# Performance work log

Hardware: AMD Instinct MI355X
Metric: run time of the kernel (lower is better)

The kernel has to match this reference:

```python
import jax, jax.numpy as jnp
import numpy as np

N = 200000
C = 256
C4 = C // 4
K = 27
B = 8
EPS = 1e-5


def setup_inputs() -> dict:
    key = jax.random.key(0)
    ks = jax.random.split(key, 16)
    s = 0.02
    inp = {
        "x": jax.random.normal(ks[0], (N, C), jnp.float32),
        "nbr6": jax.random.randint(ks[1], (N, K), 0, N + 1).astype(jnp.int32),
        "nbr12": jax.random.randint(ks[2], (N, K), 0, N + 1).astype(jnp.int32),
        "nbr18": jax.random.randint(ks[3], (N, K), 0, N + 1).astype(jnp.int32),
        "batch_idx": jnp.sort(jax.random.randint(ks[4], (N,), 0, B)).astype(jnp.int32),
        # 1x1 convs = plain matmul
        "W1": jax.random.normal(ks[5], (C, C4), jnp.float32) * s,
        "b1": jnp.zeros((C4,), jnp.float32),
        # 3^3 sparse convs: weight per kernel offset
        "W6": jax.random.normal(ks[6], (K, C, C4), jnp.float32) * s,
        "b6": jnp.zeros((C4,), jnp.float32),
        "W12": jax.random.normal(ks[7], (K, C, C4), jnp.float32) * s,
        "b12": jnp.zeros((C4,), jnp.float32),
        "W18": jax.random.normal(ks[8], (K, C, C4), jnp.float32) * s,
        "b18": jnp.zeros((C4,), jnp.float32),
        "W5": jax.random.normal(ks[9], (C, C4), jnp.float32) * s,
        "b5": jnp.zeros((C4,), jnp.float32),
        "Wc": jax.random.normal(ks[10], (5 * C4, C), jnp.float32) * s,
        "bc": jnp.zeros((C,), jnp.float32),
    }
    for i in range(1, 6):
        inp[f"g{i}"] = jnp.ones((C4,), jnp.float32)
        inp[f"be{i}"] = jnp.zeros((C4,), jnp.float32)
    inp["gc"] = jnp.ones((C,), jnp.float32)
    inp["bec"] = jnp.zeros((C,), jnp.float32)
    return inp


def _bn(x, g, b):
    # training-mode batch norm over the point dimension
    m = jnp.mean(x, axis=0)
    v = jnp.var(x, axis=0)
    return (x - m) * jax.lax.rsqrt(v + EPS) * g + b


def _sparse_conv(x, nbr, W, b):
    # gather-GEMM-scatter: x [N,C], nbr [N,K] in [0,N] (N = missing), W [K,C,Co]
    xp = jnp.concatenate([x, jnp.zeros((1, x.shape[1]), x.dtype)], axis=0)

    def step(acc, kin):
        nk, Wk = kin  # nk [N], Wk [C,Co]
        return acc + xp[nk] @ Wk, None

    init = jnp.zeros((x.shape[0], W.shape[2]), x.dtype)
    acc, _ = jax.lax.scan(step, init, (nbr.T, W))
    return acc + b


def _pool_broadcast(x, batch_idx):
    # global average pool per point cloud, broadcast back to points
    s = jax.ops.segment_sum(x, batch_idx, num_segments=B)
    cnt = jax.ops.segment_sum(jnp.ones((x.shape[0], 1), x.dtype), batch_idx, num_segments=B)
    mean = s / jnp.maximum(cnt, 1.0)
    return mean[batch_idx]


def reference(x, nbr6, nbr12, nbr18, batch_idx,
              W1, b1, W6, b6, W12, b12, W18, b18, W5, b5, Wc, bc,
              g1, be1, g2, be2, g3, be3, g4, be4, g5, be5, gc, bec):
    relu = jax.nn.relu
    x1 = relu(_bn(x @ W1 + b1, g1, be1))
    x2 = relu(_bn(_sparse_conv(x, nbr6, W6, b6), g2, be2))
    x3 = relu(_bn(_sparse_conv(x, nbr12, W12, b12), g3, be3))
    x4 = relu(_bn(_sparse_conv(x, nbr18, W18, b18), g4, be4))
    x5 = _pool_broadcast(x, batch_idx)
    x5 = relu(_bn(x5 @ W5 + b5, g5, be5))
    x6 = jnp.concatenate([x1, x2, x3, x4, x5], axis=1)
    x6 = relu(_bn(x6 @ Wc + bc, gc, bec))
    return x6 + x
```

## Files before the change

### kernel.cpp

```cpp
#include <hip/hip_runtime.h>

#define N_PTS 200000
#define KNBR 27
#define EPS_BN 1e-5f

typedef __attribute__((ext_vector_type(8))) short short8;
typedef __attribute__((ext_vector_type(4))) float f32x4;

#define WS_POOL_SUM   0u
#define WS_POOL_CNT   8192u
#define WS_BR_SUM     8448u
#define WS_BR_SQ      9472u
#define WS_C_SUM      10496u
#define WS_C_SQ       11520u
#define WS_ZROW       12544u
#define WS_A_BR       16384u
#define WS_D_BR       17408u
#define WS_AC         18432u
#define WS_DC         19456u
#define WS_R5         20480u
#define WS_WT1        24576u
#define WS_WTC        57344u
#define WS_WT6        221184u
#define WS_WT12       1105920u
#define WS_WT18       1990656u
#define WS_Y          3145728u
#define Y_STRIDE      12800000u

__device__ __forceinline__ float bf2f(unsigned short u) {
  union { unsigned int i; float f; } c; c.i = ((unsigned int)u) << 16; return c.f;
}
__device__ __forceinline__ unsigned short f2bf(float f) {
  union { float f; unsigned int i; } c; c.f = f;
  unsigned int u = c.i;
  u += 0x7fffu + ((u >> 16) & 1u);
  return (unsigned short)(u >> 16);
}
__device__ __forceinline__ short8 load8bf(const unsigned short* p) {
  return *(const short8*)p;
}

__global__ __launch_bounds__(256) void init_zero(float* __restrict__ p) {
  p[blockIdx.x * 256 + threadIdx.x] = 0.f;
}

__global__ __launch_bounds__(256) void cvt_x(
    const float* __restrict__ x, unsigned short* __restrict__ xb)
{
  size_t e = ((size_t)blockIdx.x * 256 + threadIdx.x) * 8;
  const size_t lim = (size_t)N_PTS * 256;
  if (e >= lim) {
    if (e < lim + 256) {
      short8 z = {0, 0, 0, 0, 0, 0, 0, 0};
      *(short8*)(xb + e) = z;
    }
    return;
  }
  const float4* q4 = (const float4*)(x + e);
  float4 a = q4[0], b = q4[1];
  short8 r;
  r[0] = (short)f2bf(a.x); r[1] = (short)f2bf(a.y);
  r[2] = (short)f2bf(a.z); r[3] = (short)f2bf(a.w);
  r[4] = (short)f2bf(b.x); r[5] = (short)f2bf(b.y);
  r[6] = (short)f2bf(b.z); r[7] = (short)f2bf(b.w);
  *(short8*)(xb + e) = r;
}

__global__ __launch_bounds__(256) void prep_weights(
    const float* __restrict__ W6, const float* __restrict__ W12,
    const float* __restrict__ W18, const float* __restrict__ W1,
    const float* __restrict__ Wc, char* __restrict__ ws)
{
  int slice = blockIdx.x;
  const float* src; unsigned short* dst; int R, C;
  if (slice < 27)      { src = W6  + slice * 16384;        dst = (unsigned short*)(ws + WS_WT6)  + slice * 16384;        R = 256; C = 64; }
  else if (slice < 54) { src = W12 + (slice - 27) * 16384; dst = (unsigned short*)(ws + WS_WT12) + (slice - 27) * 16384; R = 256; C = 64; }
  else if (slice < 81) { src = W18 + (slice - 54) * 16384; dst = (unsigned short*)(ws + WS_WT18) + (slice - 54) * 16384; R = 256; C = 64; }
  else if (slice == 81){ src = W1;  dst = (unsigned short*)(ws + WS_WT1); R = 256; C = 64; }
  else                 { src = Wc;  dst = (unsigned short*)(ws + WS_WTC); R = 320; C = 256; }
  int total = R * C;
  for (int e = threadIdx.x; e < total; e += 256) {
    int r = e / C, c = e - r * C;
    dst[c * R + r] = f2bf(src[e]);
  }
}

__global__ __launch_bounds__(256) void pool_kernel(
    const float* __restrict__ x, const int* __restrict__ bidx,
    float* __restrict__ pool_sum, float* __restrict__ pool_cnt)
{
  int c = threadIdx.x;
  int base = blockIdx.x * 256;
  int end = base + 256; if (end > N_PTS) end = N_PTS;
  float acc = 0.f, cnt = 0.f; int cur = -1;
  for (int row = base; row < end; ++row) {
    int b = bidx[row];
    if (b != cur) {
      if (cur >= 0) {
        atomicAdd(pool_sum + cur * 256 + c, acc);
        if (c == 0) atomicAdd(pool_cnt + cur, cnt);
      }
      acc = 0.f; cnt = 0.f; cur = b;
    }
    acc += x[(size_t)row * 256 + c];
    cnt += 1.f;
  }
  if (cur >= 0) {
    atomicAdd(pool_sum + cur * 256 + c, acc);
    if (c == 0) atomicAdd(pool_cnt + cur, cnt);
  }
}

__global__ __launch_bounds__(256) void conv_mfma(
    const unsigned short* __restrict__ xb,
    const int* __restrict__ nbr6, const int* __restrict__ nbr12,
    const int* __restrict__ nbr18, char* __restrict__ ws)
{
  const int conv = blockIdx.y;
  const int* nbr = (conv == 1) ? nbr6 : (conv == 2) ? nbr12 : (conv == 3) ? nbr18 : nullptr;
  const unsigned short* Wt = (const unsigned short*)(ws +
      (conv == 0 ? WS_WT1 : conv == 1 ? WS_WT6 : conv == 2 ? WS_WT12 : WS_WT18));
  const int kcount = conv ? KNBR : 1;
  unsigned short* yout = (unsigned short*)(ws + WS_Y) + (size_t)conv * Y_STRIDE;
  float* sum_out = (float*)(ws + WS_BR_SUM) + conv * 64;
  float* sq_out  = (float*)(ws + WS_BR_SQ)  + conv * 64;

  const int tid = threadIdx.x;
  const int wave = tid >> 6, lane = tid & 63;
  const int m = lane & 15, q = lane >> 4;
  const int base = blockIdx.x * 256 + wave * 64;

  f32x4 zero4 = {0.f, 0.f, 0.f, 0.f};
  f32x4 acc[4][4];
  #pragma unroll
  for (int a = 0; a < 4; ++a)
    #pragma unroll
    for (int b = 0; b < 4; ++b) acc[a][b] = zero4;

  int rows[4]; bool valid[4];
  #pragma unroll
  for (int ms = 0; ms < 4; ++ms) {
    rows[ms] = base + ms * 16 + m;
    valid[ms] = rows[ms] < N_PTS;
  }

  int idxc[4];
  #pragma unroll
  for (int ms = 0; ms < 4; ++ms)
    idxc[ms] = valid[ms] ? (nbr ? nbr[rows[ms] * KNBR] : rows[ms]) : N_PTS;

  #pragma unroll 1
  for (int k = 0; k < kcount; ++k) {
    int idxn[4];
    #pragma unroll
    for (int ms = 0; ms < 4; ++ms)
      idxn[ms] = (k + 1 < kcount && valid[ms]) ? nbr[rows[ms] * KNBR + k + 1] : N_PTS;

    const unsigned short* wk = Wt + (size_t)k * 16384;
    const unsigned short* ap[4];
    #pragma unroll
    for (int ms = 0; ms < 4; ++ms) ap[ms] = xb + (size_t)idxc[ms] * 256;

    #pragma unroll
    for (int cc = 0; cc < 8; ++cc) {
      const int c0 = cc * 32 + q * 8;
      short8 af[4], bfr[4];
      #pragma unroll
      for (int ms = 0; ms < 4; ++ms) af[ms] = load8bf(ap[ms] + c0);
      #pragma unroll
      for (int t = 0; t < 4; ++t) bfr[t] = load8bf(wk + (t * 16 + m) * 256 + c0);
      #pragma unroll
      for (int ms = 0; ms < 4; ++ms)
        #pragma unroll
        for (int t = 0; t < 4; ++t)
          acc[ms][t] = __builtin_amdgcn_mfma_f32_16x16x32_bf16(af[ms], bfr[t], acc[ms][t], 0, 0, 0);
    }
    #pragma unroll
    for (int ms = 0; ms < 4; ++ms) idxc[ms] = idxn[ms];
  }

  #pragma unroll
  for (int t = 0; t < 4; ++t) {
    float s = 0.f, s2 = 0.f;
    #pragma unroll
    for (int ms = 0; ms < 4; ++ms)
      #pragma unroll
      for (int r = 0; r < 4; ++r) { float v = acc[ms][t][r]; s += v; s2 += v * v; }
    s  += __shfl_xor(s, 16);  s  += __shfl_xor(s, 32);
    s2 += __shfl_xor(s2, 16); s2 += __shfl_xor(s2, 32);
    if (lane < 16) {
      atomicAdd(sum_out + t * 16 + lane, s);
      atomicAdd(sq_out  + t * 16 + lane, s2);
    }
  }

  #pragma unroll
  for (int ms = 0; ms < 4; ++ms) {
    #pragma unroll
    for (int r = 0; r < 4; ++r) {
      int row = base + ms * 16 + q * 4 + r;
      if (row < N_PTS) {
        #pragma unroll
        for (int t = 0; t < 4; ++t)
          yout[(size_t)row * 64 + t * 16 + m] = f2bf(acc[ms][t][r]);
      }
    }
  }
}

__global__ __launch_bounds__(256) void finalize_branch(
    char* __restrict__ ws,
    const float* __restrict__ g1, const float* __restrict__ be1,
    const float* __restrict__ g2, const float* __restrict__ be2,
    const float* __restrict__ g3, const float* __restrict__ be3,
    const float* __restrict__ g4, const float* __restrict__ be4,
    const float* __restrict__ g5, const float* __restrict__ be5,
    const float* __restrict__ W5)
{
  __shared__ float y5s[8][64];
  __shared__ float a5s[64], d5s[64];
  const int tid = threadIdx.x;
  float* pool_sum = (float*)(ws + WS_POOL_SUM);
  float* pool_cnt = (float*)(ws + WS_POOL_CNT);
  float* br_sum = (float*)(ws + WS_BR_SUM);
  float* br_sq  = (float*)(ws + WS_BR_SQ);
  float* a_br   = (float*)(ws + WS_A_BR);
  float* d_br   = (float*)(ws + WS_D_BR);
  unsigned short* r5 = (unsigned short*)(ws + WS_R5);

  {
    int conv = tid >> 6, co = tid & 63;
    const float* gp[4] = {g1, g2, g3, g4};
    const float* bp[4] = {be1, be2, be3, be4};
    float mean = br_sum[tid] / (float)N_PTS;
    float var = fmaxf(br_sq[tid] / (float)N_PTS - mean * mean, 0.f);
    float a = gp[conv][co] * rsqrtf(var + EPS_BN);
    a_br[tid] = a;
    d_br[tid] = bp[conv][co] - mean * a;
  }
  {
    int co = tid & 63, b0 = tid >> 6;
    for (int b = b0; b < 8; b += 4) {
      float inv = 1.f / fmaxf(pool_cnt[b], 1.f);
      float acc = 0.f;
      for (int c = 0; c < 256; ++c)
        acc += pool_sum[b * 256 + c] * inv * W5[c * 64 + co];
      y5s[b][co] = acc;
    }
  }
  __syncthreads();
  if (tid < 64) {
    int co = tid;
    float s = 0.f, s2 = 0.f;
    for (int b = 0; b < 8; ++b) {
      float cnt = pool_cnt[b], v = y5s[b][co];
      s += cnt * v; s2 += cnt * v * v;
    }
    float mean = s / (float)N_PTS;
    float var = fmaxf(s2 / (float)N_PTS - mean * mean, 0.f);
    float a = g5[co] * rsqrtf(var + EPS_BN);
    a5s[co] = a;
    d5s[co] = be5[co] - mean * a;
  }
  __syncthreads();
  for (int i = tid; i < 512; i += 256) {
    int b = i >> 6, co = i & 63;
    float v = y5s[b][co] * a5s[co] + d5s[co];
    r5[i] = f2bf(fmaxf(v, 0.f));
  }
}

__device__ __forceinline__ short8 bnrelu8(short8 v, float4 a0, float4 a1,
                                          float4 d0, float4 d1) {
  const float aa[8] = {a0.x, a0.y, a0.z, a0.w, a1.x, a1.y, a1.z, a1.w};
  const float dd[8] = {d0.x, d0.y, d0.z, d0.w, d1.x, d1.y, d1.z, d1.w};
  const unsigned short* u = (const unsigned short*)&v;
  short8 o;
  #pragma unroll
  for (int j = 0; j < 8; ++j)
    o[j] = (short)f2bf(fmaxf(bf2f(u[j]) * aa[j] + dd[j], 0.f));
  return o;
}

__global__ __launch_bounds__(256) void gemm_c(
    char* __restrict__ ws, const int* __restrict__ batch_idx,
    float* __restrict__ z)
{
  const unsigned short* y   = (const unsigned short*)(ws + WS_Y);
  const unsigned short* r5  = (const unsigned short*)(ws + WS_R5);
  const unsigned short* WtC = (const unsigned short*)(ws + WS_WTC);
  const float* a_br = (const float*)(ws + WS_A_BR);
  const float* d_br = (const float*)(ws + WS_D_BR);
  float* c_sum = (float*)(ws + WS_C_SUM);
  float* c_sq  = (float*)(ws + WS_C_SQ);

  const int tid = threadIdx.x;
  const int wave = tid >> 6, lane = tid & 63;
  const int m = lane & 15, q = lane >> 4;
  const int row0 = blockIdx.x * 64;
  const int cob = wave * 64;

  int rows[4], bb[4];
  #pragma unroll
  for (int ms = 0; ms < 4; ++ms) {
    rows[ms] = row0 + ms * 16 + m;
    bb[ms] = batch_idx[rows[ms]];
  }

  f32x4 zero4 = {0.f, 0.f, 0.f, 0.f};
  f32x4 acc[4][4];
  #pragma unroll
  for (int a = 0; a < 4; ++a)
    #pragma unroll
    for (int b = 0; b < 4; ++b) acc[a][b] = zero4;

  #pragma unroll
  for (int cc = 0; cc < 10; ++cc) {
    const int br = cc >> 1;
    const int c0 = (cc & 1) * 32 + q * 8;
    short8 af[4], bfr[4];
    if (br < 4) {
      const float* ab = a_br + br * 64 + c0;
      const float* db = d_br + br * 64 + c0;
      float4 a0 = *(const float4*)ab, a1 = *(const float4*)(ab + 4);
      float4 d0 = *(const float4*)db, d1 = *(const float4*)(db + 4);
      #pragma unroll
      for (int ms = 0; ms < 4; ++ms) {
        short8 v = load8bf(y + (size_t)br * Y_STRIDE + (size_t)rows[ms] * 64 + c0);
        af[ms] = bnrelu8(v, a0, a1, d0, d1);
      }
    } else {
      #pragma unroll
      for (int ms = 0; ms < 4; ++ms)
        af[ms] = load8bf(r5 + bb[ms] * 64 + c0);
    }
    #pragma unroll
    for (int t = 0; t < 4; ++t)
      bfr[t] = load8bf(WtC + (size_t)(cob + t * 16 + m) * 320 + cc * 32 + q * 8);
    #pragma unroll
    for (int ms = 0; ms < 4; ++ms)
      #pragma unroll
      for (int t = 0; t < 4; ++t)
        acc[ms][t] = __builtin_amdgcn_mfma_f32_16x16x32_bf16(af[ms], bfr[t], acc[ms][t], 0, 0, 0);
  }

  #pragma unroll
  for (int t = 0; t < 4; ++t) {
    float s = 0.f, s2 = 0.f;
    #pragma unroll
    for (int ms = 0; ms < 4; ++ms)
      #pragma unroll
      for (int r = 0; r < 4; ++r) { float v = acc[ms][t][r]; s += v; s2 += v * v; }
    s  += __shfl_xor(s, 16);  s  += __shfl_xor(s, 32);
    s2 += __shfl_xor(s2, 16); s2 += __shfl_xor(s2, 32);
    if (lane < 16) {
      atomicAdd(c_sum + cob + t * 16 + lane, s);
      atomicAdd(c_sq  + cob + t * 16 + lane, s2);
    }
  }

  #pragma unroll
  for (int ms = 0; ms < 4; ++ms) {
    #pragma unroll
    for (int r = 0; r < 4; ++r) {
      int row = row0 + ms * 16 + q * 4 + r;
      #pragma unroll
      for (int t = 0; t < 4; ++t)
        z[(size_t)row * 256 + cob + t * 16 + m] = acc[ms][t][r];
    }
  }
}

__global__ __launch_bounds__(256) void finalize_c(
    char* __restrict__ ws, const float* __restrict__ gc,
    const float* __restrict__ bec)
{
  int c = threadIdx.x;
  float* c_sum = (float*)(ws + WS_C_SUM);
  float* c_sq  = (float*)(ws + WS_C_SQ);
  float* ac = (float*)(ws + WS_AC);
  float* dc = (float*)(ws + WS_DC);
  float mean = c_sum[c] / (float)N_PTS;
  float var = fmaxf(c_sq[c] / (float)N_PTS - mean * mean, 0.f);
  float a = gc[c] * rsqrtf(var + EPS_BN);
  ac[c] = a;
  dc[c] = bec[c] - mean * a;
}

__global__ __launch_bounds__(256) void epilogue(
    char* __restrict__ ws, const float* __restrict__ x,
    float* __restrict__ out)
{
  size_t e = ((size_t)blockIdx.x * 256 + threadIdx.x) * 8;
  const int c = (int)(e & 255);
  const float* ac = (const float*)(ws + WS_AC);
  const float* dc = (const float*)(ws + WS_DC);
  float4 z0 = *(const float4*)(out + e);
  float4 z1 = *(const float4*)(out + e + 4);
  float4 x0 = *(const float4*)(x + e);
  float4 x1 = *(const float4*)(x + e + 4);
  float zz[8] = {z0.x, z0.y, z0.z, z0.w, z1.x, z1.y, z1.z, z1.w};
  float xx[8] = {x0.x, x0.y, x0.z, x0.w, x1.x, x1.y, x1.z, x1.w};
  #pragma unroll
  for (int j = 0; j < 8; ++j)
    zz[j] = fmaxf(zz[j] * ac[c + j] + dc[c + j], 0.f) + xx[j];
  float4 o0 = {zz[0], zz[1], zz[2], zz[3]};
  float4 o1 = {zz[4], zz[5], zz[6], zz[7]};
  *(float4*)(out + e) = o0;
  *(float4*)(out + e + 4) = o1;
}

extern "C" void kernel_launch(void* const* d_in, const int* in_sizes, int n_in,
                              void* d_out, int out_size, void* d_ws, size_t ws_size,
                              hipStream_t stream) {
  (void)in_sizes; (void)n_in; (void)out_size; (void)ws_size;
  const float* x    = (const float*)d_in[0];
  const int* nbr6   = (const int*)d_in[1];
  const int* nbr12  = (const int*)d_in[2];
  const int* nbr18  = (const int*)d_in[3];
  const int* bidx   = (const int*)d_in[4];
  const float* W1   = (const float*)d_in[5];
  const float* W6   = (const float*)d_in[7];
  const float* W12  = (const float*)d_in[9];
  const float* W18  = (const float*)d_in[11];
  const float* W5   = (const float*)d_in[13];
  const float* Wc   = (const float*)d_in[15];
  const float* g1   = (const float*)d_in[17];
  const float* be1  = (const float*)d_in[18];
  const float* g2   = (const float*)d_in[19];
  const float* be2  = (const float*)d_in[20];
  const float* g3   = (const float*)d_in[21];
  const float* be3  = (const float*)d_in[22];
  const float* g4   = (const float*)d_in[23];
  const float* be4  = (const float*)d_in[24];
  const float* g5   = (const float*)d_in[25];
  const float* be5  = (const float*)d_in[26];
  const float* gc   = (const float*)d_in[27];
  const float* bec  = (const float*)d_in[28];
  char* ws = (char*)d_ws;
  float* out = (float*)d_out;
  unsigned short* xb = (unsigned short*)d_out;

  init_zero<<<16, 256, 0, stream>>>((float*)ws);
  prep_weights<<<83, 256, 0, stream>>>(W6, W12, W18, W1, Wc, ws);
  cvt_x<<<25001, 256, 0, stream>>>(x, xb);
  pool_kernel<<<782, 256, 0, stream>>>(x, bidx,
      (float*)(ws + WS_POOL_SUM), (float*)(ws + WS_POOL_CNT));
  conv_mfma<<<dim3(782, 4), 256, 0, stream>>>(xb, nbr6, nbr12, nbr18, ws);
  finalize_branch<<<1, 256, 0, stream>>>(ws,
      g1, be1, g2, be2, g3, be3, g4, be4, g5, be5, W5);
  gemm_c<<<3125, 256, 0, stream>>>(ws, bidx, out);
  finalize_c<<<1, 256, 0, stream>>>(ws, gc, bec);
  epilogue<<<25000, 256, 0, stream>>>(ws, x, out);
}
```

Before: 2.993 ms.

## Software-pipeline gather and weight loads in sparse conv MFMA kernel with smaller tiles

Each wave now handles 32 rows instead of 64, and the grid doubles. Gathered activation fragments are prefetched four chunks ahead and weight fragments two chunks ahead across neighbor-offset boundaries, using rotating register buffers. Neighbor indices are fetched two offsets ahead, and launch bounds request 4 blocks per CU. The aim is to hide gather latency and raise occupancy, at the cost of half as much weight reuse per wave, so weight traffic per row doubles.

```diff
diff --git a/kernel.cpp b/kernel.cpp
--- a/kernel.cpp
+++ b/kernel.cpp
@@ -111,7 +111,7 @@
   }
 }
 
-__global__ __launch_bounds__(256) void conv_mfma(
+__global__ __launch_bounds__(256, 4) void conv_mfma(
     const unsigned short* __restrict__ xb,
     const int* __restrict__ nbr6, const int* __restrict__ nbr12,
     const int* __restrict__ nbr18, char* __restrict__ ws)
@@ -128,62 +128,97 @@
   const int tid = threadIdx.x;
   const int wave = tid >> 6, lane = tid & 63;
   const int m = lane & 15, q = lane >> 4;
-  const int base = blockIdx.x * 256 + wave * 64;
+  const int base = blockIdx.x * 128 + wave * 32;
+  const int qo = q * 8;
 
   f32x4 zero4 = {0.f, 0.f, 0.f, 0.f};
-  f32x4 acc[4][4];
-  #pragma unroll
-  for (int a = 0; a < 4; ++a)
+  f32x4 acc[2][4];
+  #pragma unroll
+  for (int a = 0; a < 2; ++a)
     #pragma unroll
     for (int b = 0; b < 4; ++b) acc[a][b] = zero4;
 
-  int rows[4]; bool valid[4];
-  #pragma unroll
-  for (int ms = 0; ms < 4; ++ms) {
+  int rows[2], rowK[2]; bool valid[2];
+  #pragma unroll
+  for (int ms = 0; ms < 2; ++ms) {
     rows[ms] = base + ms * 16 + m;
     valid[ms] = rows[ms] < N_PTS;
-  }
-
-  int idxc[4];
-  #pragma unroll
-  for (int ms = 0; ms < 4; ++ms)
-    idxc[ms] = valid[ms] ? (nbr ? nbr[rows[ms] * KNBR] : rows[ms]) : N_PTS;
+    rowK[ms] = rows[ms] * KNBR;
+  }
+
+  const unsigned short* ap0[2];
+  const unsigned short* ap1[2];
+  #pragma unroll
+  for (int ms = 0; ms < 2; ++ms) {
+    int i0 = valid[ms] ? (nbr ? nbr[rowK[ms]] : rows[ms]) : N_PTS;
+    int i1 = (valid[ms] && 1 < kcount) ? nbr[rowK[ms] + 1] : N_PTS;
+    ap0[ms] = xb + (size_t)i0 * 256;
+    ap1[ms] = xb + (size_t)i1 * 256;
+  }
+  const unsigned short* wk0 = Wt;
+  const unsigned short* wk1 = Wt + (size_t)(kcount > 1 ? 1 : 0) * 16384;
+
+  short8 Ab[4][2];
+  short8 Wb[2][4];
+
+  #pragma unroll
+  for (int c = 0; c < 4; ++c)
+    #pragma unroll
+    for (int ms = 0; ms < 2; ++ms)
+      Ab[c][ms] = load8bf(ap0[ms] + c * 32 + qo);
+  #pragma unroll
+  for (int c = 0; c < 2; ++c)
+    #pragma unroll
+    for (int t = 0; t < 4; ++t)
+      Wb[c][t] = load8bf(wk0 + (t * 16 + m) * 256 + c * 32 + qo);
 
   #pragma unroll 1
   for (int k = 0; k < kcount; ++k) {
-    int idxn[4];
-    #pragma unroll
-    for (int ms = 0; ms < 4; ++ms)
-      idxn[ms] = (k + 1 < kcount && valid[ms]) ? nbr[rows[ms] * KNBR + k + 1] : N_PTS;
-
-    const unsigned short* wk = Wt + (size_t)k * 16384;
-    const unsigned short* ap[4];
-    #pragma unroll
-    for (int ms = 0; ms < 4; ++ms) ap[ms] = xb + (size_t)idxc[ms] * 256;
+    int idxn[2];
+    #pragma unroll
+    for (int ms = 0; ms < 2; ++ms)
+      idxn[ms] = (valid[ms] && k + 2 < kcount) ? nbr[rowK[ms] + k + 2] : N_PTS;
+    const unsigned short* wk2 = (k + 2 < kcount) ? Wt + (size_t)(k + 2) * 16384 : wk1;
 
     #pragma unroll
     for (int cc = 0; cc < 8; ++cc) {
-      const int c0 = cc * 32 + q * 8;
-      short8 af[4], bfr[4];
-      #pragma unroll
-      for (int ms = 0; ms < 4; ++ms) af[ms] = load8bf(ap[ms] + c0);
-      #pragma unroll
-      for (int t = 0; t < 4; ++t) bfr[t] = load8bf(wk + (t * 16 + m) * 256 + c0);
-      #pragma unroll
-      for (int ms = 0; ms < 4; ++ms)
+      #pragma unroll
+      for (int ms = 0; ms < 2; ++ms)
         #pragma unroll
         for (int t = 0; t < 4; ++t)
-          acc[ms][t] = __builtin_amdgcn_mfma_f32_16x16x32_bf16(af[ms], bfr[t], acc[ms][t], 0, 0, 0);
-    }
-    #pragma unroll
-    for (int ms = 0; ms < 4; ++ms) idxc[ms] = idxn[ms];
+          acc[ms][t] = __builtin_amdgcn_mfma_f32_16x16x32_bf16(Ab[cc & 3][ms], Wb[cc & 1][t], acc[ms][t], 0, 0, 0);
+
+      {
+        const int tw = cc + 2;
+        const unsigned short* wsrc = (tw < 8) ? wk0 : wk1;
+        const int c0w = (tw & 7) * 32 + qo;
+        #pragma unroll
+        for (int t = 0; t < 4; ++t)
+          Wb[cc & 1][t] = load8bf(wsrc + (t * 16 + m) * 256 + c0w);
+      }
+      {
+        const int ta = cc + 4;
+        const int c0a = (ta & 7) * 32 + qo;
+        #pragma unroll
+        for (int ms = 0; ms < 2; ++ms)
+          Ab[cc & 3][ms] = load8bf(((ta < 8) ? ap0[ms] : ap1[ms]) + c0a);
+      }
+    }
+
+    #pragma unroll
+    for (int ms = 0; ms < 2; ++ms) {
+      ap0[ms] = ap1[ms];
+      ap1[ms] = xb + (size_t)idxn[ms] * 256;
+    }
+    wk0 = wk1;
+    wk1 = wk2;
   }
 
   #pragma unroll
   for (int t = 0; t < 4; ++t) {
     float s = 0.f, s2 = 0.f;
     #pragma unroll
-    for (int ms = 0; ms < 4; ++ms)
+    for (int ms = 0; ms < 2; ++ms)
       #pragma unroll
       for (int r = 0; r < 4; ++r) { float v = acc[ms][t][r]; s += v; s2 += v * v; }
     s  += __shfl_xor(s, 16);  s  += __shfl_xor(s, 32);
@@ -195,7 +230,7 @@
   }
 
   #pragma unroll
-  for (int ms = 0; ms < 4; ++ms) {
+  for (int ms = 0; ms < 2; ++ms) {
     #pragma unroll
     for (int r = 0; r < 4; ++r) {
       int row = base + ms * 16 + q * 4 + r;
@@ -446,7 +481,7 @@
   cvt_x<<<25001, 256, 0, stream>>>(x, xb);
   pool_kernel<<<782, 256, 0, stream>>>(x, bidx,
       (float*)(ws + WS_POOL_SUM), (float*)(ws + WS_POOL_CNT));
-  conv_mfma<<<dim3(782, 4), 256, 0, stream>>>(xb, nbr6, nbr12, nbr18, ws);
+  conv_mfma<<<dim3(1563, 4), 256, 0, stream>>>(xb, nbr6, nbr12, nbr18, ws);
   finalize_branch<<<1, 256, 0, stream>>>(ws,
       g1, be1, g2, be2, g3, be3, g4, be4, g5, be5, W5);
   gemm_c<<<3125, 256, 0, stream>>>(ws, bidx, out);
```

Result: slower. 3.951 ms (+32.0%).

## Stage per-offset conv weights in swizzled LDS instead of global loads

Applied to the files above, without the earlier changes.

The weight prep kernel now writes conv weights in an MFMA-fragment-ordered layout. The conv kernel cooperatively copies each 16K-element weight slice into shared memory, using an XOR swizzle to avoid bank conflicts. B fragments are then read from LDS rather than from global/L2. Repeated per-wave global weight traffic is replaced by one block-wide load per kernel offset, at the cost of two barriers per offset and 32KB of LDS per block, which may reduce occupancy.

```diff
diff --git a/kernel.cpp b/kernel.cpp
--- a/kernel.cpp
+++ b/kernel.cpp
@@ -72,16 +72,26 @@
     const float* __restrict__ Wc, char* __restrict__ ws)
 {
   int slice = blockIdx.x;
-  const float* src; unsigned short* dst; int R, C;
-  if (slice < 27)      { src = W6  + slice * 16384;        dst = (unsigned short*)(ws + WS_WT6)  + slice * 16384;        R = 256; C = 64; }
-  else if (slice < 54) { src = W12 + (slice - 27) * 16384; dst = (unsigned short*)(ws + WS_WT12) + (slice - 27) * 16384; R = 256; C = 64; }
-  else if (slice < 81) { src = W18 + (slice - 54) * 16384; dst = (unsigned short*)(ws + WS_WT18) + (slice - 54) * 16384; R = 256; C = 64; }
-  else if (slice == 81){ src = W1;  dst = (unsigned short*)(ws + WS_WT1); R = 256; C = 64; }
-  else                 { src = Wc;  dst = (unsigned short*)(ws + WS_WTC); R = 320; C = 256; }
-  int total = R * C;
-  for (int e = threadIdx.x; e < total; e += 256) {
-    int r = e / C, c = e - r * C;
-    dst[c * R + r] = f2bf(src[e]);
+  if (slice < 82) {
+    const float* src; unsigned short* dst;
+    if (slice < 27)      { src = W6  + slice * 16384;        dst = (unsigned short*)(ws + WS_WT6)  + slice * 16384; }
+    else if (slice < 54) { src = W12 + (slice - 27) * 16384; dst = (unsigned short*)(ws + WS_WT12) + (slice - 27) * 16384; }
+    else if (slice < 81) { src = W18 + (slice - 54) * 16384; dst = (unsigned short*)(ws + WS_WT18) + (slice - 54) * 16384; }
+    else                 { src = W1;  dst = (unsigned short*)(ws + WS_WT1); }
+    for (int e = threadIdx.x; e < 16384; e += 256) {
+      int g = e >> 3, j = e & 7;
+      int qq = g & 3, mm = (g >> 2) & 15, t = (g >> 6) & 3, cc = g >> 8;
+      int ci = cc * 32 + qq * 8 + j;
+      int co = t * 16 + mm;
+      dst[e] = f2bf(src[ci * 64 + co]);
+    }
+  } else {
+    const float* src = Wc;
+    unsigned short* dst = (unsigned short*)(ws + WS_WTC);
+    for (int e = threadIdx.x; e < 320 * 256; e += 256) {
+      int r = e >> 8, c = e & 255;
+      dst[c * 320 + r] = f2bf(src[e]);
+    }
   }
 }
 
@@ -116,6 +126,8 @@
     const int* __restrict__ nbr6, const int* __restrict__ nbr12,
     const int* __restrict__ nbr18, char* __restrict__ ws)
 {
+  __shared__ unsigned short Wlds[16384];
+
   const int conv = blockIdx.y;
   const int* nbr = (conv == 1) ? nbr6 : (conv == 2) ? nbr12 : (conv == 3) ? nbr18 : nullptr;
   const unsigned short* Wt = (const unsigned short*)(ws +
@@ -129,6 +141,9 @@
   const int wave = tid >> 6, lane = tid & 63;
   const int m = lane & 15, q = lane >> 4;
   const int base = blockIdx.x * 256 + wave * 64;
+  const int tid7 = tid & 7;
+  char* WldsB = (char*)Wlds;
+  const int rvo = ((((m * 4 + q) * 16) ^ (((m >> 1) & 7) * 16)) >> 1);
 
   f32x4 zero4 = {0.f, 0.f, 0.f, 0.f};
   f32x4 acc[4][4];
@@ -156,7 +171,18 @@
     for (int ms = 0; ms < 4; ++ms)
       idxn[ms] = (k + 1 < kcount && valid[ms]) ? nbr[rows[ms] * KNBR + k + 1] : N_PTS;
 
-    const unsigned short* wk = Wt + (size_t)k * 16384;
+    __syncthreads();
+    {
+      const unsigned short* gW = Wt + (size_t)k * 16384 + tid * 64;
+      short8 wreg[8];
+      #pragma unroll
+      for (int j = 0; j < 8; ++j) wreg[j] = load8bf(gW + j * 8);
+      #pragma unroll
+      for (int j = 0; j < 8; ++j)
+        *(short8*)(WldsB + tid * 128 + ((j ^ tid7) << 4)) = wreg[j];
+    }
+    __syncthreads();
+
     const unsigned short* ap[4];
     #pragma unroll
     for (int ms = 0; ms < 4; ++ms) ap[ms] = xb + (size_t)idxc[ms] * 256;
@@ -168,7 +194,8 @@
       #pragma unroll
       for (int ms = 0; ms < 4; ++ms) af[ms] = load8bf(ap[ms] + c0);
       #pragma unroll
-      for (int t = 0; t < 4; ++t) bfr[t] = load8bf(wk + (t * 16 + m) * 256 + c0);
+      for (int t = 0; t < 4; ++t)
+        bfr[t] = load8bf(Wlds + (cc * 4 + t) * 512 + rvo);
       #pragma unroll
       for (int ms = 0; ms < 4; ++ms)
         #pragma unroll
```

Result: faster. 2.424 ms (-19.0%).
